# Kernel tuning notes

Measured on AMD Instinct MI355X. Metric: run time of the kernel, lower is better.

Reference implementation:

```python
import jax, jax.numpy as jnp
import numpy as np


def setup_inputs() -> dict:
    key = jax.random.key(0)
    k1, k2, k3 = jax.random.split(key, 3)
    N, D_IN, D_OUT = 8192, 512, 256
    x = jax.random.normal(k1, (N, D_IN), dtype=jnp.float32)
    # binary dense adjacency (nonzero pattern is what the torch loop uses)
    adj = jax.random.randint(k2, (N, N), 0, 2, dtype=jnp.int32)
    # weight init in torch is uniform(-stdv, stdv), stdv = 1/sqrt(out_features);
    # a normal init is fine for a numerical reference
    W = jax.random.normal(k3, (D_IN, D_OUT), dtype=jnp.float32) * (1.0 / np.sqrt(D_OUT))
    return {"x": x, "adj": adj, "W": W}


def reference(x, adj, W):
    # output = X @ W  (multiply_add(self.weight, input, None) -> mm(input, weight))
    xw = jnp.matmul(x, W)  # [N, D_OUT]
    # per-node unweighted mean over neighbors given by nonzero(adj[i])
    a = (adj != 0).astype(xw.dtype)          # [N, N] binary
    deg = jnp.sum(a, axis=1, keepdims=True)  # [N, 1] neighbor counts
    out = jnp.matmul(a, xw) / deg            # D^{-1} A (X W)
    return out
```

## Files before the change

kernel.cpp:

```cpp
#include <hip/hip_runtime.h>
#include <stdint.h>

typedef __attribute__((ext_vector_type(8))) short  bf16x8;
typedef __attribute__((ext_vector_type(4))) float  f32x4;
typedef __attribute__((ext_vector_type(4))) int    int4v;
typedef __attribute__((ext_vector_type(4))) float  float4v;
typedef __attribute__((ext_vector_type(4))) unsigned int uint4v;
typedef __attribute__((ext_vector_type(2))) unsigned int uint2v;

#define NN   8192
#define DIN  512
#define DOUT 256
#define NW   (NN / 32)

#define BM2     128
#define KSPLIT2 8
#define KS2     (NN / KSPLIT2)
#define BK2     64
#define NTK     (KS2 / BK2)

#define MFMA16(a, b, c) __builtin_amdgcn_mfma_f32_16x16x32_bf16((a), (b), (c), 0, 0, 0)

__device__ __forceinline__ unsigned short f2bf(float f) {
  unsigned u = __float_as_uint(f);
  return (unsigned short)((u + 0x7FFFu + ((u >> 16) & 1u)) >> 16);
}

__device__ __forceinline__ void gld16(const void* g, void* s) {
  __builtin_amdgcn_global_load_lds(
      (const __attribute__((address_space(1))) unsigned int*)g,
      (__attribute__((address_space(3))) unsigned int*)s, 16, 0, 0);
}

__global__ void k_wt(const float* __restrict__ W, unsigned short* __restrict__ Wt) {
  int n = blockIdx.x;
  for (int c = threadIdx.x; c < DIN; c += blockDim.x)
    Wt[n * DIN + c] = f2bf(W[c * DOUT + n]);
}

__global__ __launch_bounds__(256) void k_xwt(const float* __restrict__ x,
                                             const unsigned short* __restrict__ Wt,
                                             unsigned short* __restrict__ xw_t) {
  const int mb = blockIdx.x >> 1, nb = blockIdx.x & 1;
  const int tid = threadIdx.x;
  const int w = tid >> 6, l = tid & 63;
  const int wm = w >> 1, wn = w & 1;
  const int lr = l & 15, lg = l >> 4;
  const int m_base = mb * 128 + wm * 64;
  const int n_base = nb * 128 + wn * 64;

  f32x4 acc[4][4];
  for (int i = 0; i < 4; ++i)
    for (int j = 0; j < 4; ++j) acc[i][j] = (f32x4)0.0f;

  for (int c0 = 0; c0 < DIN; c0 += 32) {
    const int c = c0 + lg * 8;
    bf16x8 af[4], bfv[4];
#pragma unroll
    for (int mt = 0; mt < 4; ++mt) {
      const float* xp = x + (size_t)(m_base + mt * 16 + lr) * DIN + c;
      float4v x0 = *reinterpret_cast<const float4v*>(xp);
      float4v x1 = *reinterpret_cast<const float4v*>(xp + 4);
      bf16x8 a;
#pragma unroll
      for (int j = 0; j < 4; ++j) {
        a[j]     = (short)f2bf(x0[j]);
        a[4 + j] = (short)f2bf(x1[j]);
      }
      af[mt] = a;
    }
#pragma unroll
    for (int nt = 0; nt < 4; ++nt)
      bfv[nt] = *reinterpret_cast<const bf16x8*>(Wt + (size_t)(n_base + nt * 16 + lr) * DIN + c);
#pragma unroll
    for (int mt = 0; mt < 4; ++mt)
#pragma unroll
      for (int nt = 0; nt < 4; ++nt)
        acc[mt][nt] = MFMA16(af[mt], bfv[nt], acc[mt][nt]);
  }

#pragma unroll
  for (int nt = 0; nt < 4; ++nt) {
    const int n = n_base + nt * 16 + lr;
#pragma unroll
    for (int mt = 0; mt < 4; ++mt) {
      const int m = m_base + mt * 16 + lg * 4;
      unsigned short b0 = f2bf(acc[mt][nt][0]), b1 = f2bf(acc[mt][nt][1]);
      unsigned short b2 = f2bf(acc[mt][nt][2]), b3 = f2bf(acc[mt][nt][3]);
      uint2v p;
      p[0] = (unsigned)b0 | ((unsigned)b1 << 16);
      p[1] = (unsigned)b2 | ((unsigned)b3 << 16);
      *reinterpret_cast<uint2v*>(xw_t + (size_t)n * NN + m) = p;
    }
  }
}

__global__ __launch_bounds__(256) void k_pack(const int* __restrict__ adj,
                                              unsigned int* __restrict__ bits,
                                              int* __restrict__ deg) {
  __shared__ int wsum[4];
  const int tid = threadIdx.x;
  const int w = tid >> 6, l = tid & 63;
  const int row = blockIdx.x;
  const int* src = adj + (size_t)row * NN + w * 2048 + l;
  unsigned long long* bdst =
      reinterpret_cast<unsigned long long*>(bits + (size_t)row * NW + w * 64);

  int cnt = 0;
#pragma unroll
  for (int it = 0; it < 32; it += 8) {
    unsigned long long b[8];
#pragma unroll
    for (int u = 0; u < 8; ++u)
      b[u] = __ballot(src[(it + u) * 64] != 0);
#pragma unroll
    for (int u = 0; u < 8; ++u) {
      if (l == 0) bdst[it + u] = b[u];
      cnt += (int)__popcll(b[u]);
    }
  }

  if (l == 0) wsum[w] = cnt;
  __syncthreads();
  if (tid == 0) deg[row] = wsum[0] + wsum[1] + wsum[2] + wsum[3];
}

__global__ __launch_bounds__(512, 4) void k_agg(const unsigned int* __restrict__ bits,
                                                const unsigned short* __restrict__ xw_t,
                                                float* __restrict__ outp) {
  __shared__ unsigned short Bs[2][16384];

  const int tid = threadIdx.x;
  const int w = tid >> 6, l = tid & 63;
  const int lr = l & 15, lg = l >> 4;
  const int wm = w >> 2, wn = w & 3;

  const int bid = blockIdx.x;
  const int ks = bid & 7;
  const int rb = bid >> 3;
  const int row0 = rb * BM2;

  const int sn = tid >> 3;
  const int sj = tid & 7;
  const unsigned short* gB = xw_t + (size_t)sn * NN + ks * KS2 + ((sj ^ (sn & 7)) * 8);

  const unsigned int* gA = bits + (size_t)(row0 + wm * 64 + lr) * NW + ks * (KS2 >> 5);

  f32x4 acc[4][4];
#pragma unroll
  for (int i = 0; i < 4; ++i)
#pragma unroll
    for (int j = 0; j < 4; ++j) acc[i][j] = (f32x4)0.0f;

  uint2v Ab[4], An[4];

#define STAGE_B(t, buf) do {                                                   \
    _Pragma("unroll")                                                          \
    for (int p_ = 0; p_ < 4; ++p_)                                             \
      gld16(gB + (size_t)p_ * 64 * NN + (t) * BK2,                             \
            (char*)&Bs[buf][0] + p_ * 8192 + w * 1024);                        \
  } while (0)

#define LOADA(t, arr) do {                                                     \
    _Pragma("unroll")                                                          \
    for (int mf_ = 0; mf_ < 4; ++mf_)                                          \
      arr[mf_] = *reinterpret_cast<const uint2v*>(gA + (size_t)mf_ * 16 * NW + 2 * (t)); \
  } while (0)

#define COMPUTE(buf) do {                                                      \
    _Pragma("unroll")                                                          \
    for (int kf_ = 0; kf_ < 2; ++kf_) {                                        \
      bf16x8 bf_[4];                                                           \
      _Pragma("unroll")                                                        \
      for (int nf_ = 0; nf_ < 4; ++nf_) {                                      \
        const int n_ = wn * 64 + nf_ * 16 + lr;                                \
        bf_[nf_] = *reinterpret_cast<const bf16x8*>(                           \
            &Bs[buf][n_ * 64 + (((kf_ * 4 + lg) ^ (n_ & 7)) * 8)]);            \
      }                                                                        \
      _Pragma("unroll")                                                        \
      for (int mf_ = 0; mf_ < 4; ++mf_) {                                      \
        const unsigned a32_ = Ab[mf_][kf_];                                    \
        uint4v q_;                                                             \
        _Pragma("unroll")                                                      \
        for (int j_ = 0; j_ < 4; ++j_) {                                       \
          unsigned b2_ = (a32_ >> (lg * 8 + 2 * j_)) & 3u;                     \
          q_[j_] = ((b2_ | (b2_ << 15)) & 0x10001u) * 0x3F80u;                 \
        }                                                                      \
        const bf16x8 af_ = *reinterpret_cast<const bf16x8*>(&q_);              \
        acc[mf_][0] = MFMA16(af_, bf_[0], acc[mf_][0]);                        \
        acc[mf_][1] = MFMA16(af_, bf_[1], acc[mf_][1]);                        \
        acc[mf_][2] = MFMA16(af_, bf_[2], acc[mf_][2]);                        \
        acc[mf_][3] = MFMA16(af_, bf_[3], acc[mf_][3]);                        \
      }                                                                        \
    }                                                                          \
  } while (0)

  STAGE_B(0, 0);
  LOADA(0, Ab);
  __syncthreads();

  for (int t = 0; t < NTK; ++t) {
    const int buf = t & 1;
    if (t + 1 < NTK) {
      STAGE_B(t + 1, buf ^ 1);
      LOADA(t + 1, An);
    }
    COMPUTE(buf);
#pragma unroll
    for (int mf = 0; mf < 4; ++mf) Ab[mf] = An[mf];
    __syncthreads();
  }
#undef STAGE_B
#undef LOADA
#undef COMPUTE

  float* po = outp + (size_t)ks * NN * DOUT;
#pragma unroll
  for (int mf = 0; mf < 4; ++mf)
#pragma unroll
    for (int nf = 0; nf < 4; ++nf)
#pragma unroll
      for (int r = 0; r < 4; ++r) {
        const int row = row0 + wm * 64 + mf * 16 + lg * 4 + r;
        const int col = wn * 64 + nf * 16 + lr;
        po[(size_t)row * DOUT + col] = acc[mf][nf][r];
      }
}

__global__ __launch_bounds__(256) void k_div(const float* __restrict__ outp,
                                             const int* __restrict__ deg,
                                             float* __restrict__ out) {
  const int idx = blockIdx.x * 256 + threadIdx.x;
  const size_t i4 = (size_t)idx * 4;
  const int row = (int)(i4 >> 8);
  float4v s = *reinterpret_cast<const float4v*>(outp + i4);
#pragma unroll
  for (int p = 1; p < KSPLIT2; ++p) {
    float4v v = *reinterpret_cast<const float4v*>(outp + (size_t)p * NN * DOUT + i4);
    s[0] += v[0]; s[1] += v[1]; s[2] += v[2]; s[3] += v[3];
  }
  const float sc = 1.0f / (float)deg[row];
  s[0] *= sc; s[1] *= sc; s[2] *= sc; s[3] *= sc;
  *reinterpret_cast<float4v*>(out + i4) = s;
}

extern "C" void kernel_launch(void* const* d_in, const int* in_sizes, int n_in,
                              void* d_out, int out_size, void* d_ws, size_t ws_size,
                              hipStream_t stream) {
  const float* x   = (const float*)d_in[0];
  const int*   adj = (const int*)d_in[1];
  const float* W   = (const float*)d_in[2];
  float* out = (float*)d_out;

  char* ws = (char*)d_ws;
  unsigned short* xw_t = (unsigned short*)ws;
  unsigned short* Wt   = (unsigned short*)(ws + (size_t)4 * 1024 * 1024);
  int*            deg  = (int*)(ws + (size_t)4 * 1024 * 1024 + 512 * 1024);
  unsigned int*   bits = (unsigned int*)(ws + (size_t)5 * 1024 * 1024);
  float*          outp = (float*)(ws + (size_t)16 * 1024 * 1024);

  k_wt<<<256, 128, 0, stream>>>(W, Wt);
  k_xwt<<<128, 256, 0, stream>>>(x, Wt, xw_t);
  k_pack<<<NN, 256, 0, stream>>>(adj, bits, deg);
  k_agg<<<(NN / BM2) * KSPLIT2, 512, 0, stream>>>(bits, xw_t, outp);
  k_div<<<(NN * DOUT) / (256 * 4), 256, 0, stream>>>(outp, deg, out);
}
```

Measured before the change: 151.5 us.

## Load aggregation B operand directly to registers, drop LDS staging and barriers

The aggregation kernel no longer stages xw_t tiles through shared memory with async global-to-LDS loads. Each wave instead loads its bf16 B fragments straight from global memory into a register double buffer. The block shrinks to 256 threads, and the grid is split over two output column halves. This removes LDS traffic and block barriers, at the cost of redundant global/L2 reads of B across waves and higher register pressure.

```diff
diff --git a/kernel.cpp b/kernel.cpp
--- a/kernel.cpp
+++ b/kernel.cpp
@@ -14,6 +14,7 @@
 #define NW   (NN / 32)
 
 #define BM2     128
+#define BN2     128
 #define KSPLIT2 8
 #define KS2     (NN / KSPLIT2)
 #define BK2     64
@@ -24,12 +25,6 @@
 __device__ __forceinline__ unsigned short f2bf(float f) {
   unsigned u = __float_as_uint(f);
   return (unsigned short)((u + 0x7FFFu + ((u >> 16) & 1u)) >> 16);
-}
-
-__device__ __forceinline__ void gld16(const void* g, void* s) {
-  __builtin_amdgcn_global_load_lds(
-      (const __attribute__((address_space(1))) unsigned int*)g,
-      (__attribute__((address_space(3))) unsigned int*)s, 16, 0, 0);
 }
 
 __global__ void k_wt(const float* __restrict__ W, unsigned short* __restrict__ Wt) {
@@ -125,26 +120,24 @@
   if (tid == 0) deg[row] = wsum[0] + wsum[1] + wsum[2] + wsum[3];
 }
 
-__global__ __launch_bounds__(512, 4) void k_agg(const unsigned int* __restrict__ bits,
+__global__ __launch_bounds__(256, 3) void k_agg(const unsigned int* __restrict__ bits,
                                                 const unsigned short* __restrict__ xw_t,
                                                 float* __restrict__ outp) {
-  __shared__ unsigned short Bs[2][16384];
-
   const int tid = threadIdx.x;
   const int w = tid >> 6, l = tid & 63;
   const int lr = l & 15, lg = l >> 4;
-  const int wm = w >> 2, wn = w & 3;
+  const int wm = w >> 1, wn = w & 1;
 
   const int bid = blockIdx.x;
   const int ks = bid & 7;
-  const int rb = bid >> 3;
+  const int rem = bid >> 3;
+  const int nb = rem & 1;
+  const int rb = rem >> 1;
   const int row0 = rb * BM2;
-
-  const int sn = tid >> 3;
-  const int sj = tid & 7;
-  const unsigned short* gB = xw_t + (size_t)sn * NN + ks * KS2 + ((sj ^ (sn & 7)) * 8);
-
-  const unsigned int* gA = bits + (size_t)(row0 + wm * 64 + lr) * NW + ks * (KS2 >> 5);
+  const int kbase = ks * KS2;
+
+  const unsigned int* gA = bits + (size_t)(row0 + wm * 64 + lr) * NW + (kbase >> 5);
+  const unsigned short* bP = xw_t + (size_t)(nb * 128 + wn * 64 + lr) * NN + kbase + lg * 8;
 
   f32x4 acc[4][4];
 #pragma unroll
@@ -152,13 +145,15 @@
 #pragma unroll
     for (int j = 0; j < 4; ++j) acc[i][j] = (f32x4)0.0f;
 
+  bf16x8 Bc[8], Bn[8];
   uint2v Ab[4], An[4];
 
-#define STAGE_B(t, buf) do {                                                   \
+#define LOADB(B, t) do {                                                       \
     _Pragma("unroll")                                                          \
-    for (int p_ = 0; p_ < 4; ++p_)                                             \
-      gld16(gB + (size_t)p_ * 64 * NN + (t) * BK2,                             \
-            (char*)&Bs[buf][0] + p_ * 8192 + w * 1024);                        \
+    for (int nf_ = 0; nf_ < 4; ++nf_) {                                        \
+      B[nf_ * 2 + 0] = *reinterpret_cast<const bf16x8*>(bP + (size_t)nf_ * 16 * NN + (t) * BK2);      \
+      B[nf_ * 2 + 1] = *reinterpret_cast<const bf16x8*>(bP + (size_t)nf_ * 16 * NN + (t) * BK2 + 32); \
+    }                                                                          \
   } while (0)
 
 #define LOADA(t, arr) do {                                                     \
@@ -167,19 +162,12 @@
       arr[mf_] = *reinterpret_cast<const uint2v*>(gA + (size_t)mf_ * 16 * NW + 2 * (t)); \
   } while (0)
 
-#define COMPUTE(buf) do {                                                      \
+#define COMPUTE(Aa, B) do {                                                    \
     _Pragma("unroll")                                                          \
     for (int kf_ = 0; kf_ < 2; ++kf_) {                                        \
-      bf16x8 bf_[4];                                                           \
-      _Pragma("unroll")                                                        \
-      for (int nf_ = 0; nf_ < 4; ++nf_) {                                      \
-        const int n_ = wn * 64 + nf_ * 16 + lr;                                \
-        bf_[nf_] = *reinterpret_cast<const bf16x8*>(                           \
-            &Bs[buf][n_ * 64 + (((kf_ * 4 + lg) ^ (n_ & 7)) * 8)]);            \
-      }                                                                        \
       _Pragma("unroll")                                                        \
       for (int mf_ = 0; mf_ < 4; ++mf_) {                                      \
-        const unsigned a32_ = Ab[mf_][kf_];                                    \
+        const unsigned a32_ = Aa[mf_][kf_];                                    \
         uint4v q_;                                                             \
         _Pragma("unroll")                                                      \
         for (int j_ = 0; j_ < 4; ++j_) {                                       \
@@ -187,30 +175,28 @@
           q_[j_] = ((b2_ | (b2_ << 15)) & 0x10001u) * 0x3F80u;                 \
         }                                                                      \
         const bf16x8 af_ = *reinterpret_cast<const bf16x8*>(&q_);              \
-        acc[mf_][0] = MFMA16(af_, bf_[0], acc[mf_][0]);                        \
-        acc[mf_][1] = MFMA16(af_, bf_[1], acc[mf_][1]);                        \
-        acc[mf_][2] = MFMA16(af_, bf_[2], acc[mf_][2]);                        \
-        acc[mf_][3] = MFMA16(af_, bf_[3], acc[mf_][3]);                        \
+        acc[mf_][0] = MFMA16(af_, B[0 * 2 + kf_], acc[mf_][0]);                \
+        acc[mf_][1] = MFMA16(af_, B[1 * 2 + kf_], acc[mf_][1]);                \
+        acc[mf_][2] = MFMA16(af_, B[2 * 2 + kf_], acc[mf_][2]);                \
+        acc[mf_][3] = MFMA16(af_, B[3 * 2 + kf_], acc[mf_][3]);                \
       }                                                                        \
     }                                                                          \
   } while (0)
 
-  STAGE_B(0, 0);
+  LOADB(Bc, 0);
   LOADA(0, Ab);
-  __syncthreads();
-
-  for (int t = 0; t < NTK; ++t) {
-    const int buf = t & 1;
-    if (t + 1 < NTK) {
-      STAGE_B(t + 1, buf ^ 1);
-      LOADA(t + 1, An);
-    }
-    COMPUTE(buf);
-#pragma unroll
-    for (int mf = 0; mf < 4; ++mf) Ab[mf] = An[mf];
-    __syncthreads();
-  }
-#undef STAGE_B
+
+  for (int t = 0; t < NTK; t += 2) {
+    LOADB(Bn, t + 1);
+    LOADA(t + 1, An);
+    COMPUTE(Ab, Bc);
+    if (t + 2 < NTK) {
+      LOADB(Bc, t + 2);
+      LOADA(t + 2, Ab);
+    }
+    COMPUTE(An, Bn);
+  }
+#undef LOADB
 #undef LOADA
 #undef COMPUTE
 
@@ -222,7 +208,7 @@
 #pragma unroll
       for (int r = 0; r < 4; ++r) {
         const int row = row0 + wm * 64 + mf * 16 + lg * 4 + r;
-        const int col = wn * 64 + nf * 16 + lr;
+        const int col = nb * 128 + wn * 64 + nf * 16 + lr;
         po[(size_t)row * DOUT + col] = acc[mf][nf][r];
       }
 }
@@ -262,6 +248,6 @@
   k_wt<<<256, 128, 0, stream>>>(W, Wt);
   k_xwt<<<128, 256, 0, stream>>>(x, Wt, xw_t);
   k_pack<<<NN, 256, 0, stream>>>(adj, bits, deg);
-  k_agg<<<(NN / BM2) * KSPLIT2, 512, 0, stream>>>(bits, xw_t, outp);
+  k_agg<<<(NN / BM2) * 2 * KSPLIT2, 256, 0, stream>>>(bits, xw_t, outp);
   k_div<<<(NN * DOUT) / (256 * 4), 256, 0, stream>>>(outp, deg, out);
 }
```

Measured after the change: 198.2 us. 30.8% more time.
